# Kernel optimization log

Measured on AMD Instinct MI355X. Metric: run time of the kernel, lower is better.

Reference implementation:

```python
import jax, jax.numpy as jnp
import numpy as np

B, C, N = 8, 64, 400  # batch, channels (in_dim), nodes


def setup_inputs() -> dict:
    key = jax.random.key(0)
    k1, k2, k3 = jax.random.split(key, 3)
    R = jax.random.normal(k1, (B, C, N, N), dtype=jnp.float32)
    W = jax.random.normal(k2, (C, C), dtype=jnp.float32) * (1.0 / np.sqrt(C))
    b = jax.random.normal(k3, (C,), dtype=jnp.float32) * 0.01
    return {"R": R, "W": W, "b": b}


def reference(R, W, b):
    # mx: (B, N, N) channel-wise max
    mx = jnp.max(R, axis=1)
    # A: relu(tanh(mx)) adjacency-like tensor (B, N, N)
    A = jax.nn.relu(jnp.tanh(mx))
    # x[b,c,k] = sum_n R[b,c,n,k] * A[b,k,n]  -> (B, C, N)
    x = jnp.einsum('bcnk,bkn->bck', R, A)
    # Linear over channel dim: y = x^T @ W^T + b, applied per node, kept as (B, C, N)
    Fg = jnp.einsum('bcn,oc->bon', x, W) + b[None, :, None]
    return Fg[..., None]  # (B, C, N, 1)
```

## Files before the change

### kernel.cpp

```cpp
#include <hip/hip_runtime.h>
#include <hip/hip_bf16.h>
#include <math.h>

#define NB 400
#define CCH 64

__global__ __launch_bounds__(256) void k1_max_tanh_T(
    const float* __restrict__ R, float* __restrict__ Tt) {
  const int b  = blockIdx.z;
  const int i0 = blockIdx.y * 64;
  const int j0 = blockIdx.x * 64;
  const int tid = threadIdx.x;
  const int tj = tid & 15;
  const int ti = tid >> 4;
  const int jbase = j0 + tj * 4;
  const int ibase = i0 + ti * 4;

  float m[4][4];
#pragma unroll
  for (int a = 0; a < 4; ++a)
#pragma unroll
    for (int d = 0; d < 4; ++d) m[a][d] = -INFINITY;

  const float* Rb = R + (size_t)b * CCH * NB * NB;
  const bool jok = (jbase < NB);

  for (int c = 0; c < CCH; ++c) {
    const float* Rc = Rb + (size_t)c * NB * NB;
#pragma unroll
    for (int a = 0; a < 4; ++a) {
      const int i = ibase + a;
      if (jok && i < NB) {
        float4 v = *reinterpret_cast<const float4*>(Rc + (size_t)i * NB + jbase);
        m[a][0] = fmaxf(m[a][0], v.x);
        m[a][1] = fmaxf(m[a][1], v.y);
        m[a][2] = fmaxf(m[a][2], v.z);
        m[a][3] = fmaxf(m[a][3], v.w);
      }
    }
  }

  __shared__ float tile[64][68];
#pragma unroll
  for (int a = 0; a < 4; ++a) {
#pragma unroll
    for (int d = 0; d < 4; ++d) {
      float t = tanhf(m[a][d]);
      t = fmaxf(t, 0.0f);
      tile[tj * 4 + d][ti * 4 + a] = t;
    }
  }
  __syncthreads();

  const int wi = tid & 15;
  const int wj = tid >> 4;
#pragma unroll
  for (int r = 0; r < 4; ++r) {
    const int jl = wj * 4 + r;
    const int jg = j0 + jl;
    const int ig = i0 + wi * 4;
    if (jg < NB && ig < NB) {
      float4 v;
      v.x = tile[jl][wi * 4 + 0];
      v.y = tile[jl][wi * 4 + 1];
      v.z = tile[jl][wi * 4 + 2];
      v.w = tile[jl][wi * 4 + 3];
      *reinterpret_cast<float4*>(Tt + ((size_t)b * NB + jg) * NB + ig) = v;
    }
  }
}

__global__ __launch_bounds__(256) void k2_reduce_n(
    const float* __restrict__ R, const float* __restrict__ Tt,
    float* __restrict__ x) {
  const int c = blockIdx.x;
  const int b = blockIdx.y;
  const int tid = threadIdx.x;
  const int half = tid >> 7;
  const int k4 = tid & 127;
  const int kk = k4 * 4;

  const float* Rbc = R + ((size_t)b * CCH + c) * NB * NB;
  const float* Ttb = Tt + (size_t)b * NB * NB;

  float4 acc = make_float4(0.f, 0.f, 0.f, 0.f);
  if (k4 < 100) {
    const int n0 = half * 200;
#pragma unroll 4
    for (int n = n0; n < n0 + 200; ++n) {
      float4 r = *reinterpret_cast<const float4*>(Rbc + (size_t)n * NB + kk);
      float4 t = *reinterpret_cast<const float4*>(Ttb + (size_t)n * NB + kk);
      acc.x += r.x * t.x;
      acc.y += r.y * t.y;
      acc.z += r.z * t.z;
      acc.w += r.w * t.w;
    }
  }

  __shared__ float4 red[128];
  if (half == 1 && k4 < 100) red[k4] = acc;
  __syncthreads();
  if (half == 0 && k4 < 100) {
    float4 o = red[k4];
    acc.x += o.x; acc.y += o.y; acc.z += o.z; acc.w += o.w;
    *reinterpret_cast<float4*>(x + ((size_t)b * CCH + c) * NB + kk) = acc;
  }
}

__global__ __launch_bounds__(256) void k3_linear(
    const float* __restrict__ x, const float* __restrict__ W,
    const float* __restrict__ bias, float* __restrict__ out) {
  const int b  = blockIdx.y;
  const int n0 = blockIdx.x * 64;
  const int tid = threadIdx.x;
  const int nl = tid & 63;
  const int og = tid >> 6;
  const int o0 = og * 16;
  const int n = n0 + nl;

  __shared__ float Ws[64][64];
  for (int idx = tid; idx < 64 * 64; idx += 256) {
    const int o = idx >> 6, c = idx & 63;
    Ws[c][o] = W[idx];
  }
  __syncthreads();

  float acc[16];
#pragma unroll
  for (int t = 0; t < 16; ++t) acc[t] = bias[o0 + t];

  if (n < NB) {
    const float* xb = x + (size_t)b * CCH * NB;
    for (int cc = 0; cc < CCH; ++cc) {
      const float xv = xb[(size_t)cc * NB + n];
#pragma unroll
      for (int q = 0; q < 4; ++q) {
        float4 w = *reinterpret_cast<const float4*>(&Ws[cc][o0 + q * 4]);
        acc[q * 4 + 0] += w.x * xv;
        acc[q * 4 + 1] += w.y * xv;
        acc[q * 4 + 2] += w.z * xv;
        acc[q * 4 + 3] += w.w * xv;
      }
    }
#pragma unroll
    for (int t = 0; t < 16; ++t) {
      out[((size_t)b * CCH + (o0 + t)) * NB + n] = acc[t];
    }
  }
}

extern "C" void kernel_launch(void* const* d_in, const int* in_sizes, int n_in,
                              void* d_out, int out_size, void* d_ws, size_t ws_size,
                              hipStream_t stream) {
  const float* R    = (const float*)d_in[0];
  const float* W    = (const float*)d_in[1];
  const float* bias = (const float*)d_in[2];
  float* out = (float*)d_out;

  float* Tt = (float*)d_ws;
  float* x  = (float*)d_ws + (size_t)8 * NB * NB;

  dim3 g1((NB + 63) / 64, (NB + 63) / 64, 8);
  k1_max_tanh_T<<<g1, 256, 0, stream>>>(R, Tt);

  dim3 g2(CCH, 8);
  k2_reduce_n<<<g2, 256, 0, stream>>>(R, Tt, x);

  dim3 g3((NB + 63) / 64, 8);
  k3_linear<<<g3, 256, 0, stream>>>(x, W, bias, out);
}
```

Baseline: 572.1 us.

## Retile max-tanh kernel to row strips and split reduction over eight slices

The channel-max kernel now gives each block a strip of four full rows, one per 128-thread group, instead of a 64x64 tile. This raises the block count from 392 to 800 and makes the reads contiguous along full rows, while the transpose goes through a small 400x5 shared tile. The reduction kernel now uses 1024 threads and splits the n-loop into eight 50-row slices combined in shared memory, which gives more memory-level parallelism for the 512-block grid. The costs are more shared-memory reduction work, possible bank conflicts on the narrow tile, and lower occupancy per block.

```diff
diff --git a/kernel.cpp b/kernel.cpp
--- a/kernel.cpp
+++ b/kernel.cpp
@@ -4,92 +4,69 @@
 
 #define NB 400
 #define CCH 64
+#define IMG ((size_t)NB * NB)
 
-__global__ __launch_bounds__(256) void k1_max_tanh_T(
+__global__ __launch_bounds__(512) void k1_max_tanh_T(
     const float* __restrict__ R, float* __restrict__ Tt) {
-  const int b  = blockIdx.z;
-  const int i0 = blockIdx.y * 64;
-  const int j0 = blockIdx.x * 64;
-  const int tid = threadIdx.x;
-  const int tj = tid & 15;
-  const int ti = tid >> 4;
-  const int jbase = j0 + tj * 4;
-  const int ibase = i0 + ti * 4;
+  const int b    = blockIdx.y;
+  const int i0   = blockIdx.x * 4;
+  const int tid  = threadIdx.x;
+  const int irow = tid >> 7;
+  const int k4   = tid & 127;
 
-  float m[4][4];
-#pragma unroll
-  for (int a = 0; a < 4; ++a)
-#pragma unroll
-    for (int d = 0; d < 4; ++d) m[a][d] = -INFINITY;
+  float4 m = make_float4(-INFINITY, -INFINITY, -INFINITY, -INFINITY);
 
-  const float* Rb = R + (size_t)b * CCH * NB * NB;
-  const bool jok = (jbase < NB);
-
-  for (int c = 0; c < CCH; ++c) {
-    const float* Rc = Rb + (size_t)c * NB * NB;
-#pragma unroll
-    for (int a = 0; a < 4; ++a) {
-      const int i = ibase + a;
-      if (jok && i < NB) {
-        float4 v = *reinterpret_cast<const float4*>(Rc + (size_t)i * NB + jbase);
-        m[a][0] = fmaxf(m[a][0], v.x);
-        m[a][1] = fmaxf(m[a][1], v.y);
-        m[a][2] = fmaxf(m[a][2], v.z);
-        m[a][3] = fmaxf(m[a][3], v.w);
-      }
+  if (k4 < 100) {
+    const float* base = R + (size_t)b * CCH * IMG + (size_t)(i0 + irow) * NB + k4 * 4;
+#pragma unroll 4
+    for (int c = 0; c < CCH; ++c) {
+      float4 v = *reinterpret_cast<const float4*>(base + (size_t)c * IMG);
+      m.x = fmaxf(m.x, v.x);
+      m.y = fmaxf(m.y, v.y);
+      m.z = fmaxf(m.z, v.z);
+      m.w = fmaxf(m.w, v.w);
     }
   }
 
-  __shared__ float tile[64][68];
-#pragma unroll
-  for (int a = 0; a < 4; ++a) {
-#pragma unroll
-    for (int d = 0; d < 4; ++d) {
-      float t = tanhf(m[a][d]);
-      t = fmaxf(t, 0.0f);
-      tile[tj * 4 + d][ti * 4 + a] = t;
-    }
+  __shared__ float tile[NB][5];
+  if (k4 < 100) {
+    tile[k4 * 4 + 0][irow] = fmaxf(tanhf(m.x), 0.0f);
+    tile[k4 * 4 + 1][irow] = fmaxf(tanhf(m.y), 0.0f);
+    tile[k4 * 4 + 2][irow] = fmaxf(tanhf(m.z), 0.0f);
+    tile[k4 * 4 + 3][irow] = fmaxf(tanhf(m.w), 0.0f);
   }
   __syncthreads();
 
-  const int wi = tid & 15;
-  const int wj = tid >> 4;
-#pragma unroll
-  for (int r = 0; r < 4; ++r) {
-    const int jl = wj * 4 + r;
-    const int jg = j0 + jl;
-    const int ig = i0 + wi * 4;
-    if (jg < NB && ig < NB) {
-      float4 v;
-      v.x = tile[jl][wi * 4 + 0];
-      v.y = tile[jl][wi * 4 + 1];
-      v.z = tile[jl][wi * 4 + 2];
-      v.w = tile[jl][wi * 4 + 3];
-      *reinterpret_cast<float4*>(Tt + ((size_t)b * NB + jg) * NB + ig) = v;
-    }
+  if (tid < NB) {
+    float4 v;
+    v.x = tile[tid][0];
+    v.y = tile[tid][1];
+    v.z = tile[tid][2];
+    v.w = tile[tid][3];
+    *reinterpret_cast<float4*>(Tt + ((size_t)b * NB + tid) * NB + i0) = v;
   }
 }
 
-__global__ __launch_bounds__(256) void k2_reduce_n(
+__global__ __launch_bounds__(1024) void k2_reduce_n(
     const float* __restrict__ R, const float* __restrict__ Tt,
     float* __restrict__ x) {
-  const int c = blockIdx.x;
-  const int b = blockIdx.y;
-  const int tid = threadIdx.x;
-  const int half = tid >> 7;
-  const int k4 = tid & 127;
-  const int kk = k4 * 4;
+  const int c     = blockIdx.x;
+  const int b     = blockIdx.y;
+  const int tid   = threadIdx.x;
+  const int slice = tid >> 7;
+  const int k4    = tid & 127;
+  const int kk    = k4 * 4;
 
-  const float* Rbc = R + ((size_t)b * CCH + c) * NB * NB;
-  const float* Ttb = Tt + (size_t)b * NB * NB;
+  const float* Rbc = R + ((size_t)b * CCH + c) * IMG + kk;
+  const float* Ttb = Tt + (size_t)b * IMG + kk;
 
   float4 acc = make_float4(0.f, 0.f, 0.f, 0.f);
   if (k4 < 100) {
-    const int n0 = half * 200;
-#pragma unroll 4
-    for (int n = n0; n < n0 + 200; ++n) {
-      float4 r = *reinterpret_cast<const float4*>(Rbc + (size_t)n * NB + kk);
-      float4 t = *reinterpret_cast<const float4*>(Ttb + (size_t)n * NB + kk);
+    const int n0 = slice * 50;
+#pragma unroll 5
+    for (int n = n0; n < n0 + 50; ++n) {
+      float4 r = *reinterpret_cast<const float4*>(Rbc + (size_t)n * NB);
+      float4 t = *reinterpret_cast<const float4*>(Ttb + (size_t)n * NB);
       acc.x += r.x * t.x;
       acc.y += r.y * t.y;
       acc.z += r.z * t.z;
@@ -97,12 +74,15 @@
     }
   }
 
-  __shared__ float4 red[128];
-  if (half == 1 && k4 < 100) red[k4] = acc;
+  __shared__ float4 red[8][100];
+  if (slice != 0 && k4 < 100) red[slice][k4] = acc;
   __syncthreads();
-  if (half == 0 && k4 < 100) {
-    float4 o = red[k4];
-    acc.x += o.x; acc.y += o.y; acc.z += o.z; acc.w += o.w;
+  if (slice == 0 && k4 < 100) {
+#pragma unroll
+    for (int s = 1; s < 8; ++s) {
+      float4 o = red[s][k4];
+      acc.x += o.x; acc.y += o.y; acc.z += o.z; acc.w += o.w;
+    }
     *reinterpret_cast<float4*>(x + ((size_t)b * CCH + c) * NB + kk) = acc;
   }
 }
@@ -158,13 +138,13 @@
   float* out = (float*)d_out;
 
   float* Tt = (float*)d_ws;
-  float* x  = (float*)d_ws + (size_t)8 * NB * NB;
+  float* x  = (float*)d_ws + (size_t)8 * IMG;
 
-  dim3 g1((NB + 63) / 64, (NB + 63) / 64, 8);
-  k1_max_tanh_T<<<g1, 256, 0, stream>>>(R, Tt);
+  dim3 g1(NB / 4, 8);
+  k1_max_tanh_T<<<g1, 512, 0, stream>>>(R, Tt);
 
   dim3 g2(CCH, 8);
-  k2_reduce_n<<<g2, 256, 0, stream>>>(R, Tt, x);
+  k2_reduce_n<<<g2, 1024, 0, stream>>>(R, Tt, x);
 
   dim3 g3((NB + 63) / 64, 8);
   k3_linear<<<g3, 256, 0, stream>>>(x, W, bias, out);
```

After: 507.3 us. 1.13x faster.
